# Kernel tuning notes

Hardware: AMD Instinct MI355X
Metric: run time of the kernel (lower is better)

The kernel has to match this reference:

```python
import jax, jax.numpy as jnp
import numpy as np

B, D, L = 8192, 2048, 4


def setup_inputs() -> dict:
    key = jax.random.key(0)
    kx, kw = jax.random.split(key)
    x = jax.random.normal(kx, (B, D), dtype=jnp.float32)
    # truncated_normal(stddev=0.01) approximated by scaled normal
    W = jax.random.normal(kw, (L, D), dtype=jnp.float32) * 0.01
    b = jnp.zeros((L, D), dtype=jnp.float32)
    return {"x": x, "W": W, "b": b}


def reference(x, W, b):
    # DCN cross layers. The original materializes the (B, d, d) outer product
    # o[b,j,k] = cross[b,j] * x0[b,k], multiplies by W[i] (broadcast over k)
    # and sums over j with keepdims. That reduces exactly to
    #   (sum_j cross[b,j]) * x0[b,k] * W[i,k]
    # so we compute the fused O(B*d) form (same math, no d^2 intermediate).
    x0 = x
    cross = x
    for i in range(W.shape[0]):
        s = jnp.sum(cross, axis=1, keepdims=True)        # (B, 1)
        cross = s * x0 * W[i] + b[i] + cross             # (B, d)
    return cross  # Flatten of (B, d) is identity
```

## Files before the change

### kernel.cpp

```cpp
#include <hip/hip_runtime.h>


typedef float v4 __attribute__((ext_vector_type(4)));

constexpr int Bn = 8192;
constexpr int D = 2048;
constexpr int L = 4;
constexpr int THREADS = 256;
constexpr int VEC = 4;
constexpr int PASSES = D / (THREADS * VEC);
constexpr int RPI = 2;
constexpr int ITERS = 2;
constexpr int RPB = RPI * ITERS;
constexpr int GRID = Bn / RPB;

__device__ inline v4 ntload(const float* p) {
    return __builtin_nontemporal_load(reinterpret_cast<const v4*>(p));
}
__device__ inline void ntstore(float* p, v4 v) {
    __builtin_nontemporal_store(v, reinterpret_cast<v4*>(p));
}
__device__ inline float hsum(v4 v) { return v.x + v.y + v.z + v.w; }

__global__ __launch_bounds__(THREADS) void cross_layer_kernel(
    const float* __restrict__ x,
    const float* __restrict__ W,
    const float* __restrict__ b,
    float* __restrict__ out)
{
    const int tid = threadIdx.x;
    const int lane = tid & 63;
    const int wid = tid >> 6;

    __shared__ float redp[4][3];
    __shared__ float red[2][4][2 * 4];

    v4 wv[L][PASSES];
    v4 bs[PASSES];
    float bred[3] = {0.f, 0.f, 0.f};

#pragma unroll
    for (int p = 0; p < PASSES; ++p) {
        const int d = p * (THREADS * VEC) + tid * VEC;
        v4 bsum = {0.f, 0.f, 0.f, 0.f};
#pragma unroll
        for (int i = 0; i < L; ++i) {
            wv[i][p] = *reinterpret_cast<const v4*>(W + i * D + d);
            v4 bb = *reinterpret_cast<const v4*>(b + i * D + d);
            bsum += bb;
            if (i < 3) bred[i] += hsum(bb);
        }
        bs[p] = bsum;
    }

#pragma unroll
    for (int k = 0; k < 3; ++k)
#pragma unroll
        for (int off = 32; off > 0; off >>= 1)
            bred[k] += __shfl_down(bred[k], off, 64);
    if (lane == 0)
#pragma unroll
        for (int k = 0; k < 3; ++k) redp[wid][k] = bred[k];
    __syncthreads();
    float Bsc[3];
#pragma unroll
    for (int k = 0; k < 3; ++k)
        Bsc[k] = redp[0][k] + redp[1][k] + redp[2][k] + redp[3][k];

    v4 xv[RPI][PASSES], xn[RPI][PASSES];
    {
        const int col = tid * VEC;
#pragma unroll
        for (int r = 0; r < RPI; ++r) {
            const float* xr = x + (size_t)(blockIdx.x + GRID * r) * D;
#pragma unroll
            for (int p = 0; p < PASSES; ++p)
                xv[r][p] = ntload(xr + p * (THREADS * VEC) + col);
        }
    }

#pragma unroll
    for (int it = 0; it < ITERS; ++it) {
        if (it + 1 < ITERS) {
            const int col = tid * VEC;
#pragma unroll
            for (int r = 0; r < RPI; ++r) {
                const float* xr = x + (size_t)(blockIdx.x + GRID * (RPI * (it + 1) + r)) * D;
#pragma unroll
                for (int p = 0; p < PASSES; ++p)
                    xn[r][p] = ntload(xr + p * (THREADS * VEC) + col);
            }
        }

        float sm[RPI * 4];
#pragma unroll
        for (int q = 0; q < RPI * 4; ++q) sm[q] = 0.f;
#pragma unroll
        for (int r = 0; r < RPI; ++r)
#pragma unroll
            for (int p = 0; p < PASSES; ++p) {
                sm[r * 4 + 0] += hsum(xv[r][p]);
#pragma unroll
                for (int i = 0; i < 3; ++i)
                    sm[r * 4 + 1 + i] += hsum(xv[r][p] * wv[i][p]);
            }

#pragma unroll
        for (int q = 0; q < RPI * 4; ++q)
#pragma unroll
            for (int off = 32; off > 0; off >>= 1)
                sm[q] += __shfl_down(sm[q], off, 64);

        if (lane == 0)
#pragma unroll
            for (int q = 0; q < RPI * 4; ++q) red[it & 1][wid][q] = sm[q];
        __syncthreads();

        float s[RPI][L];
#pragma unroll
        for (int r = 0; r < RPI; ++r) {
            const float T  = red[it & 1][0][r * 4] + red[it & 1][1][r * 4]
                           + red[it & 1][2][r * 4] + red[it & 1][3][r * 4];
            float A[3];
#pragma unroll
            for (int q = 0; q < 3; ++q)
                A[q] = red[it & 1][0][r * 4 + 1 + q] + red[it & 1][1][r * 4 + 1 + q]
                     + red[it & 1][2][r * 4 + 1 + q] + red[it & 1][3][r * 4 + 1 + q];
            s[r][0] = T;
#pragma unroll
            for (int i = 1; i < L; ++i)
                s[r][i] = s[r][i - 1] * (1.f + A[i - 1]) + Bsc[i - 1];
        }

        const int col = tid * VEC;
#pragma unroll
        for (int r = 0; r < RPI; ++r) {
            float* outr = out + (size_t)(blockIdx.x + GRID * (RPI * it + r)) * D;
#pragma unroll
            for (int p = 0; p < PASSES; ++p) {
                v4 c = {1.f, 1.f, 1.f, 1.f};
#pragma unroll
                for (int i = 0; i < L; ++i)
                    c += s[r][i] * wv[i][p];
                ntstore(outr + p * (THREADS * VEC) + col, xv[r][p] * c + bs[p]);
            }
        }

#pragma unroll
        for (int r = 0; r < RPI; ++r)
#pragma unroll
            for (int p = 0; p < PASSES; ++p)
                xv[r][p] = xn[r][p];
    }
}

extern "C" void kernel_launch(void* const* d_in, const int* in_sizes, int n_in,
                              void* d_out, int out_size, void* d_ws, size_t ws_size,
                              hipStream_t stream) {
    const float* x = (const float*)d_in[0];
    const float* W = (const float*)d_in[1];
    const float* b = (const float*)d_in[2];
    float* out = (float*)d_out;
    cross_layer_kernel<<<GRID, THREADS, 0, stream>>>(x, W, b, out);
}
```

Before: 30.26 us.

## Process one row per iteration with 8 rows per block and plain loads

Restructures the per-block loop from 2 iterations of 2 rows each to 8 iterations of 1 row each, halving the grid, and prefetches the next row while the current one is reduced and stored. The first row load is issued before the W/b setup so it overlaps that work. Nontemporal loads and stores are replaced with ordinary ones. Fewer blocks amortize W/b loading over more rows, but each block has less memory parallelism in flight and performs more barriers.

```diff
diff --git a/kernel.cpp b/kernel.cpp
--- a/kernel.cpp
+++ b/kernel.cpp
@@ -9,17 +9,9 @@
 constexpr int THREADS = 256;
 constexpr int VEC = 4;
 constexpr int PASSES = D / (THREADS * VEC);
-constexpr int RPI = 2;
-constexpr int ITERS = 2;
-constexpr int RPB = RPI * ITERS;
+constexpr int RPB = 8;
 constexpr int GRID = Bn / RPB;
 
-__device__ inline v4 ntload(const float* p) {
-    return __builtin_nontemporal_load(reinterpret_cast<const v4*>(p));
-}
-__device__ inline void ntstore(float* p, v4 v) {
-    __builtin_nontemporal_store(v, reinterpret_cast<v4*>(p));
-}
 __device__ inline float hsum(v4 v) { return v.x + v.y + v.z + v.w; }
 
 __global__ __launch_bounds__(THREADS) void cross_layer_kernel(
@@ -31,9 +23,18 @@
     const int tid = threadIdx.x;
     const int lane = tid & 63;
     const int wid = tid >> 6;
+    const int col = tid * VEC;
 
     __shared__ float redp[4][3];
-    __shared__ float red[2][4][2 * 4];
+    __shared__ float red[2][4][4];
+
+    v4 xv[PASSES], xn[PASSES];
+    {
+        const float* xr = x + (size_t)blockIdx.x * D;
+#pragma unroll
+        for (int p = 0; p < PASSES; ++p)
+            xv[p] = *reinterpret_cast<const v4*>(xr + p * (THREADS * VEC) + col);
+    }
 
     v4 wv[L][PASSES];
     v4 bs[PASSES];
@@ -41,7 +42,7 @@
 
 #pragma unroll
     for (int p = 0; p < PASSES; ++p) {
-        const int d = p * (THREADS * VEC) + tid * VEC;
+        const int d = p * (THREADS * VEC) + col;
         v4 bsum = {0.f, 0.f, 0.f, 0.f};
 #pragma unroll
         for (int i = 0; i < L; ++i) {
@@ -67,90 +68,60 @@
     for (int k = 0; k < 3; ++k)
         Bsc[k] = redp[0][k] + redp[1][k] + redp[2][k] + redp[3][k];
 
-    v4 xv[RPI][PASSES], xn[RPI][PASSES];
-    {
-        const int col = tid * VEC;
 #pragma unroll
-        for (int r = 0; r < RPI; ++r) {
-            const float* xr = x + (size_t)(blockIdx.x + GRID * r) * D;
+    for (int k = 0; k < RPB; ++k) {
+        if (k + 1 < RPB) {
+            const float* xr = x + (size_t)(blockIdx.x + GRID * (k + 1)) * D;
 #pragma unroll
             for (int p = 0; p < PASSES; ++p)
-                xv[r][p] = ntload(xr + p * (THREADS * VEC) + col);
-        }
-    }
-
-#pragma unroll
-    for (int it = 0; it < ITERS; ++it) {
-        if (it + 1 < ITERS) {
-            const int col = tid * VEC;
-#pragma unroll
-            for (int r = 0; r < RPI; ++r) {
-                const float* xr = x + (size_t)(blockIdx.x + GRID * (RPI * (it + 1) + r)) * D;
-#pragma unroll
-                for (int p = 0; p < PASSES; ++p)
-                    xn[r][p] = ntload(xr + p * (THREADS * VEC) + col);
-            }
+                xn[p] = *reinterpret_cast<const v4*>(xr + p * (THREADS * VEC) + col);
         }
 
-        float sm[RPI * 4];
+        float sm[4] = {0.f, 0.f, 0.f, 0.f};
 #pragma unroll
-        for (int q = 0; q < RPI * 4; ++q) sm[q] = 0.f;
+        for (int p = 0; p < PASSES; ++p) {
+            sm[0] += hsum(xv[p]);
 #pragma unroll
-        for (int r = 0; r < RPI; ++r)
+            for (int i = 0; i < 3; ++i)
+                sm[1 + i] += hsum(xv[p] * wv[i][p]);
+        }
 #pragma unroll
-            for (int p = 0; p < PASSES; ++p) {
-                sm[r * 4 + 0] += hsum(xv[r][p]);
-#pragma unroll
-                for (int i = 0; i < 3; ++i)
-                    sm[r * 4 + 1 + i] += hsum(xv[r][p] * wv[i][p]);
-            }
-
-#pragma unroll
-        for (int q = 0; q < RPI * 4; ++q)
+        for (int q = 0; q < 4; ++q)
 #pragma unroll
             for (int off = 32; off > 0; off >>= 1)
                 sm[q] += __shfl_down(sm[q], off, 64);
 
         if (lane == 0)
 #pragma unroll
-            for (int q = 0; q < RPI * 4; ++q) red[it & 1][wid][q] = sm[q];
+            for (int q = 0; q < 4; ++q) red[k & 1][wid][q] = sm[q];
         __syncthreads();
 
-        float s[RPI][L];
+        const float T = red[k & 1][0][0] + red[k & 1][1][0]
+                      + red[k & 1][2][0] + red[k & 1][3][0];
+        float A[3];
 #pragma unroll
-        for (int r = 0; r < RPI; ++r) {
-            const float T  = red[it & 1][0][r * 4] + red[it & 1][1][r * 4]
-                           + red[it & 1][2][r * 4] + red[it & 1][3][r * 4];
-            float A[3];
+        for (int q = 0; q < 3; ++q)
+            A[q] = red[k & 1][0][1 + q] + red[k & 1][1][1 + q]
+                 + red[k & 1][2][1 + q] + red[k & 1][3][1 + q];
+
+        float s[L];
+        s[0] = T;
 #pragma unroll
-            for (int q = 0; q < 3; ++q)
-                A[q] = red[it & 1][0][r * 4 + 1 + q] + red[it & 1][1][r * 4 + 1 + q]
-                     + red[it & 1][2][r * 4 + 1 + q] + red[it & 1][3][r * 4 + 1 + q];
-            s[r][0] = T;
+        for (int i = 1; i < L; ++i)
+            s[i] = s[i - 1] * (1.f + A[i - 1]) + Bsc[i - 1];
+
+        float* outr = out + (size_t)(blockIdx.x + GRID * k) * D;
 #pragma unroll
-            for (int i = 1; i < L; ++i)
-                s[r][i] = s[r][i - 1] * (1.f + A[i - 1]) + Bsc[i - 1];
-        }
-
-        const int col = tid * VEC;
+        for (int p = 0; p < PASSES; ++p) {
+            v4 c = {1.f, 1.f, 1.f, 1.f};
 #pragma unroll
-        for (int r = 0; r < RPI; ++r) {
-            float* outr = out + (size_t)(blockIdx.x + GRID * (RPI * it + r)) * D;
-#pragma unroll
-            for (int p = 0; p < PASSES; ++p) {
-                v4 c = {1.f, 1.f, 1.f, 1.f};
-#pragma unroll
-                for (int i = 0; i < L; ++i)
-                    c += s[r][i] * wv[i][p];
-                ntstore(outr + p * (THREADS * VEC) + col, xv[r][p] * c + bs[p]);
-            }
+            for (int i = 0; i < L; ++i)
+                c += s[i] * wv[i][p];
+            *reinterpret_cast<v4*>(outr + p * (THREADS * VEC) + col) = xv[p] * c + bs[p];
         }
 
 #pragma unroll
-        for (int r = 0; r < RPI; ++r)
-#pragma unroll
-            for (int p = 0; p < PASSES; ++p)
-                xv[r][p] = xn[r][p];
+        for (int p = 0; p < PASSES; ++p) xv[p] = xn[p];
     }
 }
 
```

Measured after the change: 26.38 us. 1.15x faster.
